# Kernel optimization log

Measured on AMD Instinct MI355X. Metric: run time of the kernel, lower is better.

## Reference

```python
import jax, jax.numpy as jnp
import numpy as np

B, TQ, TV, H = 8, 2048, 2048, 1024
LN_EPS = 1e-5


def setup_inputs() -> dict:
    key = jax.random.key(0)
    k1, k2, k3, k4 = jax.random.split(key, 4)
    query = jax.random.normal(k1, (B, TQ, H), dtype=jnp.float32)
    value = jax.random.normal(k2, (B, TV, H), dtype=jnp.float32)
    # nn.Linear(2H -> H): weight [H, 2H], bias [H]
    bound = 1.0 / np.sqrt(2 * H)
    W = jax.random.uniform(k3, (H, 2 * H), minval=-bound, maxval=bound, dtype=jnp.float32)
    b = jax.random.uniform(k4, (H,), minval=-bound, maxval=bound, dtype=jnp.float32)
    gamma = jnp.ones((H,), dtype=jnp.float32)
    beta = jnp.zeros((H,), dtype=jnp.float32)
    return {"query": query, "value": value, "W": W, "b": b, "gamma": gamma, "beta": beta}


def reference(query, value, W, b, gamma, beta):
    # scores: [B, Tq, Tv]
    score = jnp.einsum("bqh,bvh->bqv", query, value)
    attn = jax.nn.softmax(score, axis=-1)
    context = jnp.einsum("bqv,bvh->bqh", attn, value)  # [B, Tq, H]
    combined = jnp.concatenate((context, query), axis=2)  # [B, Tq, 2H]
    proj = jnp.einsum("bqk,hk->bqh", combined, W) + b  # [B, Tq, H]
    mean = jnp.mean(proj, axis=-1, keepdims=True)
    var = jnp.mean(jnp.square(proj - mean), axis=-1, keepdims=True)
    out = (proj - mean) * jax.lax.rsqrt(var + LN_EPS) * gamma + beta
    return out
```

## Files before the change

### kernel.cpp

```cpp
#include <hip/hip_runtime.h>

typedef unsigned short u16;
typedef _Float16 f16;
typedef __attribute__((ext_vector_type(8))) _Float16 f16x8;
typedef __attribute__((ext_vector_type(4))) float f32x4;

#define B_  8
#define TQ_ 2048
#define TV_ 2048
#define H_  1024

__device__ __forceinline__ u16 f2h(float x) {
    union { f16 h; u16 u; } c; c.h = (f16)x; return c.u;
}

__device__ __forceinline__ void gload_lds16(const u16* g, u16* l) {
    typedef __attribute__((address_space(1))) const unsigned short GAS;
    typedef __attribute__((address_space(3))) unsigned short LAS;
    __builtin_amdgcn_global_load_lds((GAS*)g, (LAS*)l, 16, 0, 0);
}

__global__ __launch_bounds__(256) void k_cvt(const float4* __restrict__ x,
                                             ushort4* __restrict__ o) {
    long long i = (long long)blockIdx.x * 256 + threadIdx.x;
    float4 v = x[i];
    ushort4 h;
    h.x = f2h(v.x); h.y = f2h(v.y); h.z = f2h(v.z); h.w = f2h(v.w);
    o[i] = h;
}

__global__ __launch_bounds__(256) void k_transpose(const u16* __restrict__ in,
                                                   u16* __restrict__ out) {
    __shared__ u16 s[64][65];
    const int t = threadIdx.x;
    const int c0 = blockIdx.x * 64;
    const int r0 = blockIdx.y * 64;
    const long long zb = (long long)blockIdx.z * (2048LL * 1024LL);
    const u16* ib = in + zb;
    u16* ob = out + zb;
#pragma unroll
    for (int it = 0; it < 4; ++it) {
        int rl = it * 16 + (t >> 4);
        int cl = (t & 15) * 4;
        ushort4 v = *(const ushort4*)(ib + (long long)(r0 + rl) * 1024 + c0 + cl);
        s[rl][cl + 0] = v.x; s[rl][cl + 1] = v.y; s[rl][cl + 2] = v.z; s[rl][cl + 3] = v.w;
    }
    __syncthreads();
#pragma unroll
    for (int it = 0; it < 4; ++it) {
        int cl = it * 16 + (t >> 4);
        int rl = (t & 15) * 4;
        ushort4 v;
        v.x = s[rl + 0][cl]; v.y = s[rl + 1][cl]; v.z = s[rl + 2][cl]; v.w = s[rl + 3][cl];
        *(ushort4*)(ob + (long long)(c0 + cl) * 2048 + r0 + rl) = v;
    }
}

struct GemmPass {
    const u16* A; const u16* B;
    long long sA; long long sB;
    int lda; int ldb;
};

template<int OM>
__global__ __launch_bounds__(512, 2) void k_gemm8(GemmPass p0, GemmPass p1,
                                                  int nPass, int K,
                                                  void* __restrict__ Cv, long long sC,
                                                  int ldc, const float* __restrict__ bias) {
    __shared__ __align__(16) u16 lds[65536];

    const int GX = gridDim.x;
    const int nxy = GX * gridDim.y;
    int u = blockIdx.y * GX + blockIdx.x;
    int u2 = (u & 7) * (nxy >> 3) + (u >> 3);
    const int bm = (u2 % GX) * 256;
    const int bn = (u2 / GX) * 256;
    const int z = blockIdx.z;

    const int tid = threadIdx.x;
    const int lane = tid & 63, wid = tid >> 6;
    const int wm = wid >> 2, wn = wid & 3;
    const int l16 = lane & 15, kg = lane >> 4;

    f32x4 acc[8][4];
    f32x4 zv = {0.f, 0.f, 0.f, 0.f};
#pragma unroll
    for (int i = 0; i < 8; ++i)
#pragma unroll
        for (int j = 0; j < 4; ++j) acc[i][j] = zv;

    for (int p = 0; p < nPass; ++p) {
        GemmPass ps = (p == 0) ? p0 : p1;
        const u16* Ab = ps.A + (long long)z * ps.sA;
        const u16* Bb = ps.B + (long long)z * ps.sB;
        const int lda = ps.lda, ldb = ps.ldb;
        const int NT = K >> 6;

        auto stage = [&](const u16* Xb, int ld, int R0, int k0, int h, int rbase) {
#pragma unroll
            for (int c = 0; c < 2; ++c) {
                int i = c * 512 + tid;
                int rl = i >> 3, js = i & 7;
                int r = h * 128 + rl;
                int j = js ^ (r & 7);
                gload_lds16(Xb + (long long)(R0 + r) * ld + k0 + j * 8,
                            &lds[rbase + h * 8192 + i * 8]);
            }
        };
        auto rdA = [&](int base, int mh, f16x8* dst) {
#pragma unroll
            for (int i = 0; i < 4; ++i) {
                int r = wm * 128 + mh * 64 + i * 16 + l16;
#pragma unroll
                for (int ks = 0; ks < 2; ++ks) {
                    int js = (ks * 4 + kg) ^ (r & 7);
                    dst[i * 2 + ks] = *(const f16x8*)&lds[base + r * 64 + js * 8];
                }
            }
        };
        auto rdB = [&](int base, int nh, f16x8* dst) {
#pragma unroll
            for (int jn = 0; jn < 2; ++jn) {
                int r = wn * 64 + nh * 32 + jn * 16 + l16;
#pragma unroll
                for (int ks = 0; ks < 2; ++ks) {
                    int js = (ks * 4 + kg) ^ (r & 7);
                    dst[jn * 2 + ks] = *(const f16x8*)&lds[base + r * 64 + js * 8];
                }
            }
        };

        stage(Ab, lda, bm, 0, 0, 0);
        stage(Ab, lda, bm, 0, 1, 0);
        stage(Bb, ldb, bn, 0, 0, 16384);
        stage(Bb, ldb, bn, 0, 1, 16384);
        if (NT > 1) {
            stage(Bb, ldb, bn, 64, 0, 32768 + 16384);
            stage(Bb, ldb, bn, 64, 1, 32768 + 16384);
            asm volatile("s_waitcnt vmcnt(4)" ::: "memory");
        } else {
            asm volatile("s_waitcnt vmcnt(0)" ::: "memory");
        }
        __builtin_amdgcn_s_barrier();

        f16x8 a0[8], a1[8], b0[4], b1[4];
        for (int t = 0; t < NT; ++t) {
            const int cur = t & 1;
            const int Abase = cur * 32768;
            const int Bbase = Abase + 16384;
            const int OA = (cur ^ 1) * 32768;
            const bool sa = (t + 1) < NT;
            const bool sb = (t + 2) < NT;
            rdA(Abase, 0, a0);
            rdB(Bbase, 0, b0);
            if (sa) stage(Ab, lda, bm, (t + 1) * 64, 0, OA);
            __builtin_amdgcn_s_barrier();
            __builtin_amdgcn_s_setprio(1);
#pragma unroll
            for (int i = 0; i < 4; ++i)
#pragma unroll
                for (int jn = 0; jn < 2; ++jn)
#pragma unroll
                    for (int ks = 0; ks < 2; ++ks)
                        acc[i][jn] = __builtin_amdgcn_mfma_f32_16x16x32_f16(a0[i * 2 + ks], b0[jn * 2 + ks], acc[i][jn], 0, 0, 0);
            __builtin_amdgcn_s_setprio(0);
            __builtin_amdgcn_s_barrier();
            rdB(Bbase, 1, b1);
            if (sa) stage(Ab, lda, bm, (t + 1) * 64, 1, OA);
            __builtin_amdgcn_s_barrier();
            __builtin_amdgcn_s_setprio(1);
#pragma unroll
            for (int i = 0; i < 4; ++i)
#pragma unroll
                for (int jn = 0; jn < 2; ++jn)
#pragma unroll
                    for (int ks = 0; ks < 2; ++ks)
                        acc[i][2 + jn] = __builtin_amdgcn_mfma_f32_16x16x32_f16(a0[i * 2 + ks], b1[jn * 2 + ks], acc[i][2 + jn], 0, 0, 0);
            __builtin_amdgcn_s_setprio(0);
            __builtin_amdgcn_s_barrier();
            rdA(Abase, 1, a1);
            if (sb) stage(Bb, ldb, bn, (t + 2) * 64, 0, Bbase);
            __builtin_amdgcn_s_barrier();
            __builtin_amdgcn_s_setprio(1);
#pragma unroll
            for (int i = 0; i < 4; ++i)
#pragma unroll
                for (int jn = 0; jn < 2; ++jn)
#pragma unroll
                    for (int ks = 0; ks < 2; ++ks)
                        acc[4 + i][2 + jn] = __builtin_amdgcn_mfma_f32_16x16x32_f16(a1[i * 2 + ks], b1[jn * 2 + ks], acc[4 + i][2 + jn], 0, 0, 0);
            __builtin_amdgcn_s_setprio(0);
            __builtin_amdgcn_s_barrier();
            if (sb) {
                stage(Bb, ldb, bn, (t + 2) * 64, 1, Bbase);
                asm volatile("s_waitcnt vmcnt(4)" ::: "memory");
            } else if (sa) {
                asm volatile("s_waitcnt vmcnt(0)" ::: "memory");
            }
            __builtin_amdgcn_s_barrier();
            __builtin_amdgcn_s_setprio(1);
#pragma unroll
            for (int i = 0; i < 4; ++i)
#pragma unroll
                for (int jn = 0; jn < 2; ++jn)
#pragma unroll
                    for (int ks = 0; ks < 2; ++ks)
                        acc[4 + i][jn] = __builtin_amdgcn_mfma_f32_16x16x32_f16(a1[i * 2 + ks], b0[jn * 2 + ks], acc[4 + i][jn], 0, 0, 0);
            __builtin_amdgcn_s_setprio(0);
            __builtin_amdgcn_s_barrier();
        }
    }

    const int colBase = bn + wn * 64;
    const int rowBase = bm + wm * 128;
#pragma unroll
    for (int mi = 0; mi < 8; ++mi) {
#pragma unroll
        for (int nj = 0; nj < 4; ++nj) {
            int col = colBase + nj * 16 + l16;
            float badd = bias ? bias[col] : 0.f;
#pragma unroll
            for (int r = 0; r < 4; ++r) {
                long long row = rowBase + mi * 16 + kg * 4 + r;
                long long idx = (long long)z * sC + row * (long long)ldc + col;
                float vv = acc[mi][nj][r] + badd;
                if constexpr (OM == 1) ((u16*)Cv)[idx] = f2h(vv);
                else ((float*)Cv)[idx] = vv;
            }
        }
    }
}

__global__ __launch_bounds__(256) void k_softmax(float* __restrict__ S) {
    long long rowi = (long long)blockIdx.y * TQ_ + blockIdx.x;
    float* row = S + rowi * TV_;
    u16* prow = (u16*)row;
    int t = threadIdx.x;
    float4 a = *(const float4*)(row + t * 4);
    float4 c = *(const float4*)(row + 1024 + t * 4);
    float m = fmaxf(fmaxf(fmaxf(a.x, a.y), fmaxf(a.z, a.w)),
                    fmaxf(fmaxf(c.x, c.y), fmaxf(c.z, c.w)));
#pragma unroll
    for (int o = 32; o; o >>= 1) m = fmaxf(m, __shfl_xor(m, o));
    __shared__ float rm[4], rs[4];
    if ((t & 63) == 0) rm[t >> 6] = m;
    __syncthreads();
    m = fmaxf(fmaxf(rm[0], rm[1]), fmaxf(rm[2], rm[3]));
    float e0 = __expf(a.x - m), e1 = __expf(a.y - m), e2 = __expf(a.z - m), e3 = __expf(a.w - m);
    float e4 = __expf(c.x - m), e5 = __expf(c.y - m), e6 = __expf(c.z - m), e7 = __expf(c.w - m);
    float s = ((e0 + e1) + (e2 + e3)) + ((e4 + e5) + (e6 + e7));
#pragma unroll
    for (int o = 32; o; o >>= 1) s += __shfl_xor(s, o);
    if ((t & 63) == 0) rs[t >> 6] = s;
    __syncthreads();
    s = rs[0] + rs[1] + rs[2] + rs[3];
    float inv = 1.f / s;
    ushort4 o0, o1;
    o0.x = f2h(e0 * inv); o0.y = f2h(e1 * inv); o0.z = f2h(e2 * inv); o0.w = f2h(e3 * inv);
    o1.x = f2h(e4 * inv); o1.y = f2h(e5 * inv); o1.z = f2h(e6 * inv); o1.w = f2h(e7 * inv);
    __syncthreads();
    *(ushort4*)(prow + t * 4) = o0;
    *(ushort4*)(prow + 1024 + t * 4) = o1;
}

__global__ __launch_bounds__(256) void k_layernorm(float* __restrict__ O,
                                                   const float* __restrict__ g,
                                                   const float* __restrict__ b) {
    float* row = O + (long long)blockIdx.x * H_;
    int t = threadIdx.x;
    float4 x = *(const float4*)(row + t * 4);
    float s1 = x.x + x.y + x.z + x.w;
    float s2 = x.x * x.x + x.y * x.y + x.z * x.z + x.w * x.w;
#pragma unroll
    for (int o = 32; o; o >>= 1) { s1 += __shfl_xor(s1, o); s2 += __shfl_xor(s2, o); }
    __shared__ float r1[4], r2[4];
    if ((t & 63) == 0) { r1[t >> 6] = s1; r2[t >> 6] = s2; }
    __syncthreads();
    s1 = r1[0] + r1[1] + r1[2] + r1[3];
    s2 = r2[0] + r2[1] + r2[2] + r2[3];
    float mean = s1 * (1.f / H_);
    float var = s2 * (1.f / H_) - mean * mean;
    float rstd = rsqrtf(fmaxf(var, 0.f) + 1e-5f);
    float4 gv = *(const float4*)(g + t * 4);
    float4 bv = *(const float4*)(b + t * 4);
    float4 o;
    o.x = (x.x - mean) * rstd * gv.x + bv.x;
    o.y = (x.y - mean) * rstd * gv.y + bv.y;
    o.z = (x.z - mean) * rstd * gv.z + bv.z;
    o.w = (x.w - mean) * rstd * gv.w + bv.w;
    *(float4*)(row + t * 4) = o;
}

extern "C" void kernel_launch(void* const* d_in, const int* in_sizes, int n_in,
                              void* d_out, int out_size, void* d_ws, size_t ws_size,
                              hipStream_t stream) {
    const float* q     = (const float*)d_in[0];
    const float* v     = (const float*)d_in[1];
    const float* W     = (const float*)d_in[2];
    const float* bias  = (const float*)d_in[3];
    const float* gamma = (const float*)d_in[4];
    const float* beta  = (const float*)d_in[5];
    float* out = (float*)d_out;
    char* ws = (char*)d_ws;

    const long long nQV = (long long)B_ * TQ_ * H_;
    const long long nW  = (long long)H_ * 2 * H_;

    u16* Qh = (u16*)ws;
    u16* Vh = Qh + nQV;
    u16* VT = Vh + nQV;
    u16* Cb = VT + nQV;
    u16* Wh = Cb + nQV;
    char* dyn = (char*)(Wh + nW);
    size_t fixedBytes = (size_t)(dyn - ws);
    const size_t perZ = (size_t)TQ_ * TV_ * 4;

    int Z = 1;
    for (int cand = 8; cand >= 1; cand >>= 1) {
        if (fixedBytes + (size_t)cand * perZ <= ws_size) { Z = cand; break; }
    }
    float* S = (float*)dyn;

    k_cvt<<<dim3(nQV / 4 / 256), dim3(256), 0, stream>>>((const float4*)q, (ushort4*)Qh);
    k_cvt<<<dim3(nQV / 4 / 256), dim3(256), 0, stream>>>((const float4*)v, (ushort4*)Vh);
    k_cvt<<<dim3(nW / 4 / 256),  dim3(256), 0, stream>>>((const float4*)W, (ushort4*)Wh);
    k_transpose<<<dim3(H_ / 64, TV_ / 64, B_), dim3(256), 0, stream>>>(Vh, VT);

    for (int c0 = 0; c0 < B_; c0 += Z) {
        const long long ob = (long long)c0 * TQ_ * H_;
        GemmPass s0{Qh + ob, Vh + ob, (long long)TQ_ * H_, (long long)TV_ * H_, H_, H_};
        k_gemm8<0><<<dim3(TQ_ / 256, TV_ / 256, Z), dim3(512), 0, stream>>>(
            s0, s0, 1, H_, S, (long long)TQ_ * TV_, TV_, nullptr);
        k_softmax<<<dim3(TQ_, Z), dim3(256), 0, stream>>>(S);
        GemmPass pv{(const u16*)S, VT + (long long)c0 * H_ * TV_,
                    2048LL * 4096LL, (long long)H_ * TV_, 4096, TV_};
        k_gemm8<1><<<dim3(TQ_ / 256, H_ / 256, Z), dim3(512), 0, stream>>>(
            pv, pv, 1, TV_, Cb + ob, (long long)TQ_ * H_, H_, nullptr);
    }

    GemmPass j0{Cb, Wh,      0, 0, H_, 2 * H_};
    GemmPass j1{Qh, Wh + H_, 0, 0, H_, 2 * H_};
    k_gemm8<0><<<dim3(B_ * TQ_ / 256, H_ / 256, 1), dim3(512), 0, stream>>>(
        j0, j1, 2, H_, out, 0, H_, bias);

    k_layernorm<<<dim3(B_ * TQ_), dim3(256), 0, stream>>>(out, gamma, beta);
}
```

Before: 384.9 us.

## Restructure attention pipeline: fused convert-transpose, concat buffer, batched PV GEMM

Fuses the V fp16 conversion with the transpose, and writes Q straight into the right half of a concatenated [context|query] buffer so the final projection becomes a single K=2048 GEMM. Softmax now writes fp16 probabilities to a separate full-batch buffer, which lets the PV GEMM run once over all batches instead of per chunk. The QK GEMM uses a new 256x128 tile variant with a 1D swizzled grid, processing two batches per launch. It removes launches, extra passes over V and the chunk loop, at the cost of a much larger workspace (the full fp16 P matrix) and more work per softmax launch.

```diff
diff --git a/kernel.cpp b/kernel.cpp
--- a/kernel.cpp
+++ b/kernel.cpp
@@ -29,30 +29,44 @@
     o[i] = h;
 }
 
-__global__ __launch_bounds__(256) void k_transpose(const u16* __restrict__ in,
-                                                   u16* __restrict__ out) {
+__global__ __launch_bounds__(256) void k_cvt_q(const float4* __restrict__ q4,
+                                               u16* __restrict__ CQ) {
+    long long i = (long long)blockIdx.x * 256 + threadIdx.x;
+    float4 x = q4[i];
+    ushort4 h;
+    h.x = f2h(x.x); h.y = f2h(x.y); h.z = f2h(x.z); h.w = f2h(x.w);
+    long long row = i >> 8;
+    int col = (int)(i & 255) * 4;
+    *(ushort4*)(CQ + row * 2048 + 1024 + col) = h;
+}
+
+__global__ __launch_bounds__(256) void k_cvt_vt(const float* __restrict__ v,
+                                                u16* __restrict__ Vh,
+                                                u16* __restrict__ VT) {
     __shared__ u16 s[64][65];
     const int t = threadIdx.x;
     const int c0 = blockIdx.x * 64;
     const int r0 = blockIdx.y * 64;
     const long long zb = (long long)blockIdx.z * (2048LL * 1024LL);
-    const u16* ib = in + zb;
-    u16* ob = out + zb;
+    const float* ib = v + zb;
 #pragma unroll
     for (int it = 0; it < 4; ++it) {
         int rl = it * 16 + (t >> 4);
         int cl = (t & 15) * 4;
-        ushort4 v = *(const ushort4*)(ib + (long long)(r0 + rl) * 1024 + c0 + cl);
-        s[rl][cl + 0] = v.x; s[rl][cl + 1] = v.y; s[rl][cl + 2] = v.z; s[rl][cl + 3] = v.w;
+        float4 x = *(const float4*)(ib + (long long)(r0 + rl) * 1024 + c0 + cl);
+        ushort4 h;
+        h.x = f2h(x.x); h.y = f2h(x.y); h.z = f2h(x.z); h.w = f2h(x.w);
+        *(ushort4*)(Vh + zb + (long long)(r0 + rl) * 1024 + c0 + cl) = h;
+        s[rl][cl + 0] = h.x; s[rl][cl + 1] = h.y; s[rl][cl + 2] = h.z; s[rl][cl + 3] = h.w;
     }
     __syncthreads();
 #pragma unroll
     for (int it = 0; it < 4; ++it) {
         int cl = it * 16 + (t >> 4);
         int rl = (t & 15) * 4;
-        ushort4 v;
-        v.x = s[rl + 0][cl]; v.y = s[rl + 1][cl]; v.z = s[rl + 2][cl]; v.w = s[rl + 3][cl];
-        *(ushort4*)(ob + (long long)(c0 + cl) * 2048 + r0 + rl) = v;
+        ushort4 o;
+        o.x = s[rl + 0][cl]; o.y = s[rl + 1][cl]; o.z = s[rl + 2][cl]; o.w = s[rl + 3][cl];
+        *(ushort4*)(VT + zb + (long long)(c0 + cl) * 2048 + r0 + rl) = o;
     }
 }
 
@@ -62,95 +76,95 @@
     int lda; int ldb;
 };
 
-template<int OM>
-__global__ __launch_bounds__(512, 2) void k_gemm8(GemmPass p0, GemmPass p1,
-                                                  int nPass, int K,
+template<int NH, int OM>
+__global__ __launch_bounds__(512, 2) void k_gemm8(GemmPass p0,
+                                                  int K, int mnTiles, int gn,
                                                   void* __restrict__ Cv, long long sC,
                                                   int ldc, const float* __restrict__ bias) {
-    __shared__ __align__(16) u16 lds[65536];
-
-    const int GX = gridDim.x;
-    const int nxy = GX * gridDim.y;
-    int u = blockIdx.y * GX + blockIdx.x;
-    int u2 = (u & 7) * (nxy >> 3) + (u >> 3);
-    const int bm = (u2 % GX) * 256;
-    const int bn = (u2 / GX) * 256;
-    const int z = blockIdx.z;
+    constexpr int BUFU = 16384 + NH * 8192;
+    __shared__ __align__(16) u16 lds[2 * BUFU];
+
+    const int nper = gridDim.x >> 3;
+    const int g = (blockIdx.x & 7) * nper + (blockIdx.x >> 3);
+    const int z = g / mnTiles;
+    const int rem = g - z * mnTiles;
+    const int bm = (rem / gn) * 256;
+    const int bn = (rem % gn) * (NH * 128);
 
     const int tid = threadIdx.x;
     const int lane = tid & 63, wid = tid >> 6;
     const int wm = wid >> 2, wn = wid & 3;
     const int l16 = lane & 15, kg = lane >> 4;
 
-    f32x4 acc[8][4];
+    f32x4 acc[8][NH * 2];
     f32x4 zv = {0.f, 0.f, 0.f, 0.f};
 #pragma unroll
     for (int i = 0; i < 8; ++i)
 #pragma unroll
-        for (int j = 0; j < 4; ++j) acc[i][j] = zv;
-
-    for (int p = 0; p < nPass; ++p) {
-        GemmPass ps = (p == 0) ? p0 : p1;
-        const u16* Ab = ps.A + (long long)z * ps.sA;
-        const u16* Bb = ps.B + (long long)z * ps.sB;
-        const int lda = ps.lda, ldb = ps.ldb;
-        const int NT = K >> 6;
-
-        auto stage = [&](const u16* Xb, int ld, int R0, int k0, int h, int rbase) {
-#pragma unroll
-            for (int c = 0; c < 2; ++c) {
-                int i = c * 512 + tid;
-                int rl = i >> 3, js = i & 7;
-                int r = h * 128 + rl;
-                int j = js ^ (r & 7);
-                gload_lds16(Xb + (long long)(R0 + r) * ld + k0 + j * 8,
-                            &lds[rbase + h * 8192 + i * 8]);
+        for (int j = 0; j < NH * 2; ++j) acc[i][j] = zv;
+
+    const u16* Ab = p0.A + (long long)z * p0.sA;
+    const u16* Bb = p0.B + (long long)z * p0.sB;
+    const int lda = p0.lda, ldb = p0.ldb;
+    const int NT = K >> 6;
+
+    auto stage = [&](const u16* Xb, int ld, int R0, int k0, int h, int rbase) {
+#pragma unroll
+        for (int c = 0; c < 2; ++c) {
+            int i = c * 512 + tid;
+            int rl = i >> 3, js = i & 7;
+            int r = h * 128 + rl;
+            int j = js ^ (r & 7);
+            gload_lds16(Xb + (long long)(R0 + r) * ld + k0 + j * 8,
+                        &lds[rbase + h * 8192 + i * 8]);
+        }
+    };
+    auto rdA = [&](int base, int mh, f16x8* dst) {
+#pragma unroll
+        for (int i = 0; i < 4; ++i) {
+            int r = wm * 128 + mh * 64 + i * 16 + l16;
+#pragma unroll
+            for (int ks = 0; ks < 2; ++ks) {
+                int js = (ks * 4 + kg) ^ (r & 7);
+                dst[i * 2 + ks] = *(const f16x8*)&lds[base + r * 64 + js * 8];
             }
-        };
-        auto rdA = [&](int base, int mh, f16x8* dst) {
-#pragma unroll
-            for (int i = 0; i < 4; ++i) {
-                int r = wm * 128 + mh * 64 + i * 16 + l16;
-#pragma unroll
-                for (int ks = 0; ks < 2; ++ks) {
-                    int js = (ks * 4 + kg) ^ (r & 7);
-                    dst[i * 2 + ks] = *(const f16x8*)&lds[base + r * 64 + js * 8];
-                }
+        }
+    };
+    auto rdB = [&](int base, int nh, f16x8* dst) {
+#pragma unroll
+        for (int jn = 0; jn < 2; ++jn) {
+            int r = wn * (NH * 32) + nh * 32 + jn * 16 + l16;
+#pragma unroll
+            for (int ks = 0; ks < 2; ++ks) {
+                int js = (ks * 4 + kg) ^ (r & 7);
+                dst[jn * 2 + ks] = *(const f16x8*)&lds[base + r * 64 + js * 8];
             }
-        };
-        auto rdB = [&](int base, int nh, f16x8* dst) {
-#pragma unroll
-            for (int jn = 0; jn < 2; ++jn) {
-                int r = wn * 64 + nh * 32 + jn * 16 + l16;
-#pragma unroll
-                for (int ks = 0; ks < 2; ++ks) {
-                    int js = (ks * 4 + kg) ^ (r & 7);
-                    dst[jn * 2 + ks] = *(const f16x8*)&lds[base + r * 64 + js * 8];
-                }
-            }
-        };
-
-        stage(Ab, lda, bm, 0, 0, 0);
-        stage(Ab, lda, bm, 0, 1, 0);
-        stage(Bb, ldb, bn, 0, 0, 16384);
-        stage(Bb, ldb, bn, 0, 1, 16384);
-        if (NT > 1) {
-            stage(Bb, ldb, bn, 64, 0, 32768 + 16384);
-            stage(Bb, ldb, bn, 64, 1, 32768 + 16384);
-            asm volatile("s_waitcnt vmcnt(4)" ::: "memory");
-        } else {
-            asm volatile("s_waitcnt vmcnt(0)" ::: "memory");
         }
-        __builtin_amdgcn_s_barrier();
-
-        f16x8 a0[8], a1[8], b0[4], b1[4];
-        for (int t = 0; t < NT; ++t) {
-            const int cur = t & 1;
-            const int Abase = cur * 32768;
-            const int Bbase = Abase + 16384;
-            const int OA = (cur ^ 1) * 32768;
-            const bool sa = (t + 1) < NT;
-            const bool sb = (t + 2) < NT;
+    };
+
+    stage(Ab, lda, bm, 0, 0, 0);
+    stage(Ab, lda, bm, 0, 1, 0);
+#pragma unroll
+    for (int h = 0; h < NH; ++h) stage(Bb, ldb, bn, 0, h, 16384);
+    if (NT > 1) {
+#pragma unroll
+        for (int h = 0; h < NH; ++h) stage(Bb, ldb, bn, 64, h, BUFU + 16384);
+        if constexpr (NH == 2) asm volatile("s_waitcnt vmcnt(4)" ::: "memory");
+        else                   asm volatile("s_waitcnt vmcnt(2)" ::: "memory");
+    } else {
+        asm volatile("s_waitcnt vmcnt(0)" ::: "memory");
+    }
+    __builtin_amdgcn_s_barrier();
+
+    f16x8 a0[8], a1[8], b0[4], b1[4];
+    for (int t = 0; t < NT; ++t) {
+        const int cur = t & 1;
+        const int Abase = cur * BUFU;
+        const int Bbase = Abase + 16384;
+        const int OA = (cur ^ 1) * BUFU;
+        const bool sa = (t + 1) < NT;
+        const bool sb = (t + 2) < NT;
+        if constexpr (NH == 2) {
             rdA(Abase, 0, a0);
             rdB(Bbase, 0, b0);
             if (sa) stage(Ab, lda, bm, (t + 1) * 64, 0, OA);
@@ -208,15 +222,49 @@
                         acc[4 + i][jn] = __builtin_amdgcn_mfma_f32_16x16x32_f16(a1[i * 2 + ks], b0[jn * 2 + ks], acc[4 + i][jn], 0, 0, 0);
             __builtin_amdgcn_s_setprio(0);
             __builtin_amdgcn_s_barrier();
+        } else {
+            rdA(Abase, 0, a0);
+            rdB(Bbase, 0, b0);
+            if (sa) stage(Ab, lda, bm, (t + 1) * 64, 0, OA);
+            __builtin_amdgcn_s_barrier();
+            __builtin_amdgcn_s_setprio(1);
+#pragma unroll
+            for (int i = 0; i < 4; ++i)
+#pragma unroll
+                for (int jn = 0; jn < 2; ++jn)
+#pragma unroll
+                    for (int ks = 0; ks < 2; ++ks)
+                        acc[i][jn] = __builtin_amdgcn_mfma_f32_16x16x32_f16(a0[i * 2 + ks], b0[jn * 2 + ks], acc[i][jn], 0, 0, 0);
+            __builtin_amdgcn_s_setprio(0);
+            __builtin_amdgcn_s_barrier();
+            rdA(Abase, 1, a1);
+            if (sa) stage(Ab, lda, bm, (t + 1) * 64, 1, OA);
+            if (sb) {
+                stage(Bb, ldb, bn, (t + 2) * 64, 0, Bbase);
+                asm volatile("s_waitcnt vmcnt(2)" ::: "memory");
+            } else if (sa) {
+                asm volatile("s_waitcnt vmcnt(0)" ::: "memory");
+            }
+            __builtin_amdgcn_s_barrier();
+            __builtin_amdgcn_s_setprio(1);
+#pragma unroll
+            for (int i = 0; i < 4; ++i)
+#pragma unroll
+                for (int jn = 0; jn < 2; ++jn)
+#pragma unroll
+                    for (int ks = 0; ks < 2; ++ks)
+                        acc[4 + i][jn] = __builtin_amdgcn_mfma_f32_16x16x32_f16(a1[i * 2 + ks], b0[jn * 2 + ks], acc[4 + i][jn], 0, 0, 0);
+            __builtin_amdgcn_s_setprio(0);
+            __builtin_amdgcn_s_barrier();
         }
     }
 
-    const int colBase = bn + wn * 64;
+    const int colBase = bn + wn * (NH * 32);
     const int rowBase = bm + wm * 128;
 #pragma unroll
     for (int mi = 0; mi < 8; ++mi) {
 #pragma unroll
-        for (int nj = 0; nj < 4; ++nj) {
+        for (int nj = 0; nj < NH * 2; ++nj) {
             int col = colBase + nj * 16 + l16;
             float badd = bias ? bias[col] : 0.f;
 #pragma unroll
@@ -231,10 +279,19 @@
     }
 }
 
-__global__ __launch_bounds__(256) void k_softmax(float* __restrict__ S) {
-    long long rowi = (long long)blockIdx.y * TQ_ + blockIdx.x;
-    float* row = S + rowi * TV_;
-    u16* prow = (u16*)row;
+__global__ __launch_bounds__(256) void k_softmax(const float* __restrict__ S,
+                                                 u16* __restrict__ P, int mode) {
+    int q, zc;
+    if (mode == 2) {
+        int x = blockIdx.x & 7;
+        zc = x >> 2;
+        q = ((x & 3) << 9) | (blockIdx.x >> 3);
+    } else {
+        zc = 0;
+        q = blockIdx.x;
+    }
+    const float* row = S + ((long long)zc * TQ_ + q) * TV_;
+    u16* prow = P + ((long long)zc * TQ_ + q) * TV_;
     int t = threadIdx.x;
     float4 a = *(const float4*)(row + t * 4);
     float4 c = *(const float4*)(row + 1024 + t * 4);
@@ -258,7 +315,6 @@
     ushort4 o0, o1;
     o0.x = f2h(e0 * inv); o0.y = f2h(e1 * inv); o0.z = f2h(e2 * inv); o0.w = f2h(e3 * inv);
     o1.x = f2h(e4 * inv); o1.y = f2h(e5 * inv); o1.z = f2h(e6 * inv); o1.w = f2h(e7 * inv);
-    __syncthreads();
     *(ushort4*)(prow + t * 4) = o0;
     *(ushort4*)(prow + 1024 + t * 4) = o1;
 }
@@ -305,43 +361,41 @@
 
     const long long nQV = (long long)B_ * TQ_ * H_;
     const long long nW  = (long long)H_ * 2 * H_;
-
-    u16* Qh = (u16*)ws;
-    u16* Vh = Qh + nQV;
+    const long long nCQ = (long long)B_ * TQ_ * 2048;
+    const long long nP  = (long long)B_ * TQ_ * TV_;
+
+    u16* Vh = (u16*)ws;
     u16* VT = Vh + nQV;
-    u16* Cb = VT + nQV;
-    u16* Wh = Cb + nQV;
-    char* dyn = (char*)(Wh + nW);
-    size_t fixedBytes = (size_t)(dyn - ws);
+    u16* Wh = VT + nQV;
+    u16* CQ = Wh + nW;
+    u16* Pa = CQ + nCQ;
+    float* S = (float*)(Pa + nP);
+    size_t fixedBytes = (size_t)((char*)S - ws);
     const size_t perZ = (size_t)TQ_ * TV_ * 4;
 
-    int Z = 1;
-    for (int cand = 8; cand >= 1; cand >>= 1) {
-        if (fixedBytes + (size_t)cand * perZ <= ws_size) { Z = cand; break; }
-    }
-    float* S = (float*)dyn;
-
-    k_cvt<<<dim3(nQV / 4 / 256), dim3(256), 0, stream>>>((const float4*)q, (ushort4*)Qh);
-    k_cvt<<<dim3(nQV / 4 / 256), dim3(256), 0, stream>>>((const float4*)v, (ushort4*)Vh);
-    k_cvt<<<dim3(nW / 4 / 256),  dim3(256), 0, stream>>>((const float4*)W, (ushort4*)Wh);
-    k_transpose<<<dim3(H_ / 64, TV_ / 64, B_), dim3(256), 0, stream>>>(Vh, VT);
-
-    for (int c0 = 0; c0 < B_; c0 += Z) {
-        const long long ob = (long long)c0 * TQ_ * H_;
-        GemmPass s0{Qh + ob, Vh + ob, (long long)TQ_ * H_, (long long)TV_ * H_, H_, H_};
-        k_gemm8<0><<<dim3(TQ_ / 256, TV_ / 256, Z), dim3(512), 0, stream>>>(
-            s0, s0, 1, H_, S, (long long)TQ_ * TV_, TV_, nullptr);
-        k_softmax<<<dim3(TQ_, Z), dim3(256), 0, stream>>>(S);
-        GemmPass pv{(const u16*)S, VT + (long long)c0 * H_ * TV_,
-                    2048LL * 4096LL, (long long)H_ * TV_, 4096, TV_};
-        k_gemm8<1><<<dim3(TQ_ / 256, H_ / 256, Z), dim3(512), 0, stream>>>(
-            pv, pv, 1, TV_, Cb + ob, (long long)TQ_ * H_, H_, nullptr);
-    }
-
-    GemmPass j0{Cb, Wh,      0, 0, H_, 2 * H_};
-    GemmPass j1{Qh, Wh + H_, 0, 0, H_, 2 * H_};
-    k_gemm8<0><<<dim3(B_ * TQ_ / 256, H_ / 256, 1), dim3(512), 0, stream>>>(
-        j0, j1, 2, H_, out, 0, H_, bias);
+    int Zc = (fixedBytes + 2 * perZ <= ws_size) ? 2 : 1;
+
+    k_cvt_q<<<dim3(nQV / 4 / 256), dim3(256), 0, stream>>>((const float4*)q, CQ);
+    k_cvt  <<<dim3(nW / 4 / 256),  dim3(256), 0, stream>>>((const float4*)W, (ushort4*)Wh);
+    k_cvt_vt<<<dim3(H_ / 64, TV_ / 64, B_), dim3(256), 0, stream>>>(v, Vh, VT);
+
+    for (int c0 = 0; c0 < B_; c0 += Zc) {
+        GemmPass s0{CQ + (long long)c0 * TQ_ * 2048 + 1024,
+                    Vh + (long long)c0 * TV_ * H_,
+                    (long long)TQ_ * 2048, (long long)TV_ * H_, 2048, H_};
+        k_gemm8<1, 0><<<dim3(Zc * 128), dim3(512), 0, stream>>>(
+            s0, H_, 128, 16, S, (long long)TQ_ * TV_, TV_, nullptr);
+        k_softmax<<<dim3(Zc * TQ_), dim3(256), 0, stream>>>(
+            S, Pa + (long long)c0 * TQ_ * TV_, Zc);
+    }
+
+    GemmPass pv{Pa, VT, (long long)TQ_ * TV_, (long long)H_ * TV_, TV_, TV_};
+    k_gemm8<2, 1><<<dim3(256), dim3(512), 0, stream>>>(
+        pv, TV_, 32, 4, CQ, (long long)TQ_ * 2048, 2048, nullptr);
+
+    GemmPass j0{CQ, Wh, 0, 0, 2048, 2 * H_};
+    k_gemm8<2, 0><<<dim3(256), dim3(512), 0, stream>>>(
+        j0, 2 * H_, 256, 4, out, 0, H_, bias);
 
     k_layernorm<<<dim3(B_ * TQ_), dim3(256), 0, stream>>>(out, gamma, beta);
 }
```

After: 352.2 us. 8.5% less time.
